# Kernel optimization log

Hardware: AMD Instinct MI355X
Metric: run time of the kernel (lower is better)

Reference implementation:

```python
import jax, jax.numpy as jnp
import numpy as np


def setup_inputs() -> dict:
    key = jax.random.key(0)
    kx, ky = jax.random.split(key)
    B, N, D = 16, 2048, 128
    x = jax.random.normal(kx, (B, N, D), dtype=jnp.float32)
    y = jax.random.normal(ky, (B, N, D), dtype=jnp.float32)
    return {"x": x, "y": y}


def reference(x, y):
    # Pairwise squared-Euclidean cost: out[b, i, j] = sum_d (x[b,i,d] - y[b,j,d])**2
    # Computed via ||x||^2 + ||y||^2 - 2 <x, y> to avoid the O(N^2 D) intermediate
    # that the original repeat/view pattern materializes.
    x2 = jnp.sum(x * x, axis=-1)                      # [B, N]
    y2 = jnp.sum(y * y, axis=-1)                      # [B, N]
    xy = jnp.einsum('bid,bjd->bij', x, y)             # [B, N, N]
    cost = x2[:, :, None] + y2[:, None, :] - 2.0 * xy  # [B, N, N]
    return jnp.maximum(cost, 0.0)
```

## Files before the change

kernel.cpp:

```cpp
#include <hip/hip_runtime.h>


#define Bb   16
#define Nn   2048
#define Dd   128
#define TILE 128
#define JT   8

typedef __bf16 bf16x8 __attribute__((ext_vector_type(8)));
typedef float  f32x4  __attribute__((ext_vector_type(4)));

__device__ __forceinline__ bf16x8 pack8(float4 a, float4 b) {
  bf16x8 r;
  r[0] = (__bf16)a.x; r[1] = (__bf16)a.y; r[2] = (__bf16)a.z; r[3] = (__bf16)a.w;
  r[4] = (__bf16)b.x; r[5] = (__bf16)b.y; r[6] = (__bf16)b.z; r[7] = (__bf16)b.w;
  return r;
}

__global__ __launch_bounds__(256, 2)
void pairwise_cost_kernel(const float* __restrict__ x,
                          const float* __restrict__ y,
                          float* __restrict__ out) {
  __shared__ float yn_s[TILE * JT];

  const int t  = threadIdx.x;
  const int b  = blockIdx.z;
  const int i0 = blockIdx.y * TILE;
  const int j0 = blockIdx.x * (TILE * JT);

  const int w    = t >> 6;
  const int lane = t & 63;
  const int lrow = lane & 15;
  const int quad = lane >> 4;
  const int ib   = (w >> 1) * 64;
  const int jb   = (w & 1) * 64;

  {
    const int r2 = t >> 1, half = t & 1;
    for (int g = 0; g < JT; ++g) {
      const float4* src =
          (const float4*)(y + ((size_t)b * Nn + j0 + g * TILE + r2) * Dd + half * 64);
      float ss = 0.f;
      #pragma unroll
      for (int q = 0; q < 16; ++q) {
        float4 v = src[q];
        ss += v.x * v.x + v.y * v.y + v.z * v.z + v.w * v.w;
      }
      ss += __shfl_xor(ss, 1);
      if (half == 0) yn_s[g * TILE + r2] = ss;
    }
  }

  bf16x8 xf[4][4];
  float  xn[4];
  {
    const float* xb = x + ((size_t)b * Nn + i0 + ib) * Dd;
    #pragma unroll
    for (int ti = 0; ti < 4; ++ti) {
      const float* rp = xb + (ti * 16 + lrow) * Dd + quad * 8;
      float ss = 0.f;
      #pragma unroll
      for (int k = 0; k < 4; ++k) {
        float4 u0 = *(const float4*)(rp + k * 32);
        float4 u1 = *(const float4*)(rp + k * 32 + 4);
        ss += u0.x * u0.x + u0.y * u0.y + u0.z * u0.z + u0.w * u0.w
            + u1.x * u1.x + u1.y * u1.y + u1.z * u1.z + u1.w * u1.w;
        xf[ti][k] = pack8(u0, u1);
      }
      ss += __shfl_xor(ss, 16);
      ss += __shfl_xor(ss, 32);
      xn[ti] = ss;
    }
  }
  __syncthreads();

  float* outb = out + (size_t)b * Nn * Nn;

  for (int jt = 0; jt < JT; ++jt) {
    bf16x8 yf[4][4];
    {
      const float* ybase = y + ((size_t)b * Nn + j0 + jt * TILE) * Dd;
      #pragma unroll
      for (int k = 0; k < 4; ++k)
        #pragma unroll
        for (int tj = 0; tj < 4; ++tj) {
          const float* rp = ybase + (jb + tj * 16 + lrow) * Dd + k * 32 + quad * 8;
          float4 u0 = *(const float4*)(rp);
          float4 u1 = *(const float4*)(rp + 4);
          yf[k][tj] = pack8(u0, u1);
        }
    }

    f32x4 acc[4][4];
    #pragma unroll
    for (int ti = 0; ti < 4; ++ti)
      #pragma unroll
      for (int tj = 0; tj < 4; ++tj)
        acc[ti][tj] = (f32x4){0.f, 0.f, 0.f, 0.f};

    #pragma unroll
    for (int k = 0; k < 4; ++k)
      #pragma unroll
      for (int ti = 0; ti < 4; ++ti)
        #pragma unroll
        for (int tj = 0; tj < 4; ++tj)
          acc[ti][tj] = __builtin_amdgcn_mfma_f32_16x16x32_bf16(yf[k][tj], xf[ti][k],
                                                               acc[ti][tj], 0, 0, 0);

    #pragma unroll
    for (int ti = 0; ti < 4; ++ti) {
      const size_t orow =
          (size_t)(i0 + ib + ti * 16 + lrow) * Nn + (j0 + jt * TILE + jb);
      const float xnv = xn[ti];
      #pragma unroll
      for (int tj = 0; tj < 4; ++tj) {
        f32x4 yn4 = *(const f32x4*)&yn_s[jt * TILE + jb + tj * 16 + quad * 4];
        f32x4 a   = acc[ti][tj];
        f32x4 c;
        #pragma unroll
        for (int rg = 0; rg < 4; ++rg)
          c[rg] = fmaxf(xnv + yn4[rg] - 2.0f * a[rg], 0.0f);
        __builtin_nontemporal_store(c, (f32x4*)(outb + orow + tj * 16 + quad * 4));
      }
    }
  }
}

extern "C" void kernel_launch(void* const* d_in, const int* in_sizes, int n_in,
                              void* d_out, int out_size, void* d_ws, size_t ws_size,
                              hipStream_t stream) {
  const float* x = (const float*)d_in[0];
  const float* y = (const float*)d_in[1];
  float* out = (float*)d_out;
  dim3 grid(Nn / (TILE * JT), Nn / TILE, Bb);
  pairwise_cost_kernel<<<grid, dim3(256, 1, 1), 0, stream>>>(x, y, out);
}
```

Measured before the change: 381.5 us.

## Use small 64x128 tiles per block, fuse y-norm into fragment loads

Replaces the large 128x1024 per-block tile, which looped over eight j-subtiles, with one 64x128 output tile per block, giving a much larger grid and higher occupancy (launch bounds 4). The y squared norms are now taken from the same loads that build the MFMA fragments and reduced with shuffles, which removes the shared-memory prepass and the barrier. Nontemporal stores become plain stores. In exchange, x and y tiles are reloaded from global memory more often, though L2 should absorb most of that.

```diff
diff --git a/kernel.cpp b/kernel.cpp
--- a/kernel.cpp
+++ b/kernel.cpp
@@ -1,11 +1,11 @@
 #include <hip/hip_runtime.h>
 
 
-#define Bb   16
-#define Nn   2048
-#define Dd   128
-#define TILE 128
-#define JT   8
+#define Bb 16
+#define Nn 2048
+#define Dd 128
+#define BM 64
+#define BN 128
 
 typedef __bf16 bf16x8 __attribute__((ext_vector_type(8)));
 typedef float  f32x4  __attribute__((ext_vector_type(4)));
@@ -17,46 +17,28 @@
   return r;
 }
 
-__global__ __launch_bounds__(256, 2)
+__global__ __launch_bounds__(256, 4)
 void pairwise_cost_kernel(const float* __restrict__ x,
                           const float* __restrict__ y,
                           float* __restrict__ out) {
-  __shared__ float yn_s[TILE * JT];
-
   const int t  = threadIdx.x;
   const int b  = blockIdx.z;
-  const int i0 = blockIdx.y * TILE;
-  const int j0 = blockIdx.x * (TILE * JT);
+  const int i0 = blockIdx.y * BM;
+  const int j0 = blockIdx.x * BN;
 
   const int w    = t >> 6;
   const int lane = t & 63;
   const int lrow = lane & 15;
   const int quad = lane >> 4;
-  const int ib   = (w >> 1) * 64;
+  const int ib   = (w >> 1) * 32;
   const int jb   = (w & 1) * 64;
 
-  {
-    const int r2 = t >> 1, half = t & 1;
-    for (int g = 0; g < JT; ++g) {
-      const float4* src =
-          (const float4*)(y + ((size_t)b * Nn + j0 + g * TILE + r2) * Dd + half * 64);
-      float ss = 0.f;
-      #pragma unroll
-      for (int q = 0; q < 16; ++q) {
-        float4 v = src[q];
-        ss += v.x * v.x + v.y * v.y + v.z * v.z + v.w * v.w;
-      }
-      ss += __shfl_xor(ss, 1);
-      if (half == 0) yn_s[g * TILE + r2] = ss;
-    }
-  }
-
-  bf16x8 xf[4][4];
-  float  xn[4];
+  bf16x8 xf[2][4];
+  float  xn[2];
   {
     const float* xb = x + ((size_t)b * Nn + i0 + ib) * Dd;
     #pragma unroll
-    for (int ti = 0; ti < 4; ++ti) {
+    for (int ti = 0; ti < 2; ++ti) {
       const float* rp = xb + (ti * 16 + lrow) * Dd + quad * 8;
       float ss = 0.f;
       #pragma unroll
@@ -72,56 +54,67 @@
       xn[ti] = ss;
     }
   }
-  __syncthreads();
+
+  f32x4 acc[2][4];
+  #pragma unroll
+  for (int ti = 0; ti < 2; ++ti)
+    #pragma unroll
+    for (int tj = 0; tj < 4; ++tj)
+      acc[ti][tj] = (f32x4){0.f, 0.f, 0.f, 0.f};
+
+  float ssy[4] = {0.f, 0.f, 0.f, 0.f};
+  {
+    const float* yb = y + ((size_t)b * Nn + j0 + jb) * Dd;
+    #pragma unroll
+    for (int k = 0; k < 4; ++k) {
+      bf16x8 yf[4];
+      #pragma unroll
+      for (int tj = 0; tj < 4; ++tj) {
+        const float* rp = yb + (tj * 16 + lrow) * Dd + k * 32 + quad * 8;
+        float4 u0 = *(const float4*)(rp);
+        float4 u1 = *(const float4*)(rp + 4);
+        ssy[tj] += u0.x * u0.x + u0.y * u0.y + u0.z * u0.z + u0.w * u0.w
+                 + u1.x * u1.x + u1.y * u1.y + u1.z * u1.z + u1.w * u1.w;
+        yf[tj] = pack8(u0, u1);
+      }
+      #pragma unroll
+      for (int ti = 0; ti < 2; ++ti)
+        #pragma unroll
+        for (int tj = 0; tj < 4; ++tj)
+          acc[ti][tj] = __builtin_amdgcn_mfma_f32_16x16x32_bf16(yf[tj], xf[ti][k],
+                                                               acc[ti][tj], 0, 0, 0);
+    }
+  }
+
+  float yn[4];
+  #pragma unroll
+  for (int tj = 0; tj < 4; ++tj) {
+    float s = ssy[tj];
+    s += __shfl_xor(s, 16);
+    s += __shfl_xor(s, 32);
+    yn[tj] = s;
+  }
+
+  f32x4 yn4[4];
+  #pragma unroll
+  for (int tj = 0; tj < 4; ++tj)
+    #pragma unroll
+    for (int rg = 0; rg < 4; ++rg)
+      yn4[tj][rg] = __shfl(yn[tj], quad * 4 + rg);
 
   float* outb = out + (size_t)b * Nn * Nn;
-
-  for (int jt = 0; jt < JT; ++jt) {
-    bf16x8 yf[4][4];
-    {
-      const float* ybase = y + ((size_t)b * Nn + j0 + jt * TILE) * Dd;
+  #pragma unroll
+  for (int ti = 0; ti < 2; ++ti) {
+    const size_t orow = (size_t)(i0 + ib + ti * 16 + lrow) * Nn + (j0 + jb);
+    const float  xnv  = xn[ti];
+    #pragma unroll
+    for (int tj = 0; tj < 4; ++tj) {
+      f32x4 a = acc[ti][tj];
+      f32x4 c;
       #pragma unroll
-      for (int k = 0; k < 4; ++k)
-        #pragma unroll
-        for (int tj = 0; tj < 4; ++tj) {
-          const float* rp = ybase + (jb + tj * 16 + lrow) * Dd + k * 32 + quad * 8;
-          float4 u0 = *(const float4*)(rp);
-          float4 u1 = *(const float4*)(rp + 4);
-          yf[k][tj] = pack8(u0, u1);
-        }
-    }
-
-    f32x4 acc[4][4];
-    #pragma unroll
-    for (int ti = 0; ti < 4; ++ti)
-      #pragma unroll
-      for (int tj = 0; tj < 4; ++tj)
-        acc[ti][tj] = (f32x4){0.f, 0.f, 0.f, 0.f};
-
-    #pragma unroll
-    for (int k = 0; k < 4; ++k)
-      #pragma unroll
-      for (int ti = 0; ti < 4; ++ti)
-        #pragma unroll
-        for (int tj = 0; tj < 4; ++tj)
-          acc[ti][tj] = __builtin_amdgcn_mfma_f32_16x16x32_bf16(yf[k][tj], xf[ti][k],
-                                                               acc[ti][tj], 0, 0, 0);
-
-    #pragma unroll
-    for (int ti = 0; ti < 4; ++ti) {
-      const size_t orow =
-          (size_t)(i0 + ib + ti * 16 + lrow) * Nn + (j0 + jt * TILE + jb);
-      const float xnv = xn[ti];
-      #pragma unroll
-      for (int tj = 0; tj < 4; ++tj) {
-        f32x4 yn4 = *(const f32x4*)&yn_s[jt * TILE + jb + tj * 16 + quad * 4];
-        f32x4 a   = acc[ti][tj];
-        f32x4 c;
-        #pragma unroll
-        for (int rg = 0; rg < 4; ++rg)
-          c[rg] = fmaxf(xnv + yn4[rg] - 2.0f * a[rg], 0.0f);
-        __builtin_nontemporal_store(c, (f32x4*)(outb + orow + tj * 16 + quad * 4));
-      }
+      for (int rg = 0; rg < 4; ++rg)
+        c[rg] = fmaxf(xnv + yn4[tj][rg] - 2.0f * a[rg], 0.0f);
+      *(f32x4*)(outb + orow + tj * 16 + quad * 4) = c;
     }
   }
 }
@@ -132,6 +125,6 @@
   const float* x = (const float*)d_in[0];
   const float* y = (const float*)d_in[1];
   float* out = (float*)d_out;
-  dim3 grid(Nn / (TILE * JT), Nn / TILE, Bb);
+  dim3 grid(Nn / BN, Nn / BM, Bb);
   pairwise_cost_kernel<<<grid, dim3(256, 1, 1), 0, stream>>>(x, y, out);
 }
```

Result: slower. 432.0 us (+13.2%).
